# Performance work log

Measured on AMD Instinct MI355X. Metric: run time of the kernel, lower is better.

## Reference

```python
import jax, jax.numpy as jnp
import numpy as np

NUM_SEGMENTS = 8
SHIFT_DIV = 4
DEFORM_GROUPS = 2


def conv1d(x, w, b):
    # x: [N, C, T], w: [O, I, K], padding=1 (same)
    y = jax.lax.conv_general_dilated(x, w, window_strides=(1,), padding=[(1, 1)],
                                     dimension_numbers=('NCH', 'OIH', 'NCH'))
    return y + b[None, :, None]


def linear_sampler(data, offset, weight):
    # data: [N, T, C, H, W]; offset: [N, 1] or [N, T]; weight: [N, T]
    n, t = data.shape[0], data.shape[1]
    location = jnp.arange(1, t + 1, dtype=data.dtype)          # [T]
    off = offset + location                                    # [N, T]
    f = jnp.floor(off).astype(jnp.int32)
    o0 = jnp.clip(f, 0, t + 1)
    o1 = jnp.clip(f + 1, 0, t + 1)
    pad = jnp.pad(data, ((0, 0), (1, 1), (0, 0), (0, 0), (0, 0)))  # [N, T+2, C, H, W]
    d0 = jnp.take_along_axis(pad, o0[:, :, None, None, None], axis=1)
    d1 = jnp.take_along_axis(pad, o1[:, :, None, None, None], axis=1)
    w0 = (1.0 - (off - o0.astype(data.dtype)))[:, :, None, None, None]
    return (w0 * d0 + (1.0 - w0) * d1) * weight[:, :, None, None, None]


def setup_inputs() -> dict:
    key = jax.random.key(0)
    ks = jax.random.split(key, 8)
    n, c, h, w = 64, 256, 56, 56
    ns = NUM_SEGMENTS
    in_ch = c // SHIFT_DIV  # 64, channels fed to offset/weight nets
    x = jax.random.normal(ks[0], (n, c, h, w), dtype=jnp.float32)
    s = 0.05
    return {
        'x': x,
        'conv_off_w': jax.random.normal(ks[1], (1, in_ch, 3), jnp.float32) * s,
        'conv_off_b': jnp.zeros((1,), jnp.float32),
        'fc1_w': jax.random.normal(ks[2], (ns, ns), jnp.float32) * s,
        'fc1_b': jnp.zeros((ns,), jnp.float32),
        'fc2_w': jax.random.normal(ks[3], (DEFORM_GROUPS, ns), jnp.float32) * s,
        'fc2_b': jnp.full((DEFORM_GROUPS,), 0.5108, jnp.float32),
        'conv_wt_w': jax.random.normal(ks[4], (DEFORM_GROUPS, in_ch, 3), jnp.float32) * s,
        'conv_wt_b': jnp.zeros((DEFORM_GROUPS,), jnp.float32),
    }


def reference(x, conv_off_w, conv_off_b, fc1_w, fc1_b, fc2_w, fc2_b, conv_wt_w, conv_wt_b):
    n, c, h, w = x.shape
    ns = NUM_SEGMENTS
    nb = n // ns
    num_folds = c // SHIFT_DIV
    x_unchanged = x[:, num_folds:]
    xd = x[:, :num_folds].reshape(nb, ns, num_folds, h, w)
    # global spatial pool -> [nb, num_folds, ns]
    x_pooled = xd.mean(axis=(3, 4)).transpose(0, 2, 1)
    # OffsetNet: conv1d -> fc1 -> relu -> fc2 -> 4*(sigmoid-0.5)
    xo = conv1d(x_pooled, conv_off_w, conv_off_b).reshape(nb, ns)
    xo = jax.nn.relu(xo @ fc1_w.T + fc1_b)
    xo = xo @ fc2_w.T + fc2_b                       # [nb, groups]
    x_offset = (4.0 * (jax.nn.sigmoid(xo) - 0.5)).reshape(nb, 1, DEFORM_GROUPS)
    # WeightNet: conv1d -> 2*sigmoid
    xw = conv1d(x_pooled, conv_wt_w, conv_wt_b)     # [nb, groups, ns]
    x_weight = 2.0 * jax.nn.sigmoid(xw.transpose(0, 2, 1))  # [nb, ns, groups]
    x_offset = -x_offset
    fi = num_folds // DEFORM_GROUPS // 2
    parts = []
    for i in range(DEFORM_GROUPS):
        parts.append(linear_sampler(xd[:, :, i * fi:(i + 1) * fi],
                                    x_offset[:, :, i], x_weight[:, :, i]))
    for i in range(DEFORM_GROUPS):
        p = i + DEFORM_GROUPS
        parts.append(linear_sampler(xd[:, :, p * fi:(p + 1) * fi],
                                    -x_offset[:, :, i], x_weight[:, :, i]))
    x_shift = jnp.concatenate(parts, axis=2)        # [nb, ns, num_folds, h, w]
    x_shift = x_shift.reshape(n, num_folds, h, w)
    x_out = jnp.concatenate([x_shift, x_unchanged], axis=1)
    return x_out, x_offset, x_weight
```

## Files before the change

kernel.cpp:

```cpp
#include <hip/hip_runtime.h>
#include <hip/hip_bf16.h>


#define HW4      784
#define N_TOT    64
#define C_TOT    256
#define FOLDS    64
#define MAIN_OUT (64u*256u*784u)
#define OFF_OUT  51380224
#define WT_OUT   51380240

typedef float v4f __attribute__((ext_vector_type(4)));

__global__ __launch_bounds__(256) void pool_kernel(const v4f* __restrict__ x,
                                                   float* __restrict__ pool) {
    const int p = blockIdx.x;
    const int n = p >> 6, f = p & 63;
    const v4f* base = x + (size_t)(n * C_TOT + f) * HW4;
    float s = 0.f;
    for (int i = threadIdx.x; i < HW4; i += 256) {
        v4f v = base[i];
        s += (v.x + v.y) + (v.z + v.w);
    }
    for (int m = 32; m >= 1; m >>= 1) s += __shfl_xor(s, m, 64);
    __shared__ float ls[4];
    if ((threadIdx.x & 63) == 0) ls[threadIdx.x >> 6] = s;
    __syncthreads();
    if (threadIdx.x == 0)
        pool[p] = (ls[0] + ls[1] + ls[2] + ls[3]) * (1.0f / 3136.0f);
}

__global__ __launch_bounds__(256) void mid_kernel(const float* __restrict__ pool,
    const float* __restrict__ cow, const float* __restrict__ cob,
    const float* __restrict__ f1w, const float* __restrict__ f1b,
    const float* __restrict__ f2w, const float* __restrict__ f2b,
    const float* __restrict__ cww, const float* __restrict__ cwb,
    float* __restrict__ out_off, float* __restrict__ out_wt,
    v4f* __restrict__ param) {
    __shared__ float sp[4096];
    __shared__ float sxo[64];
    __shared__ float sxw[128];
    __shared__ float sy[64];
    __shared__ float soff[16];
    __shared__ float swt[128];
    const int t = threadIdx.x;
    for (int i = t; i < 4096; i += 256) sp[i] = pool[i];
    __syncthreads();
    if (t < 64) {
        const int b = t >> 3, s = t & 7;
        float acc = cob[0];
        for (int f = 0; f < 64; ++f) {
            float vm = (s >= 1) ? sp[(b*8 + s - 1)*64 + f] : 0.f;
            float v0 = sp[(b*8 + s)*64 + f];
            float vp = (s <= 6) ? sp[(b*8 + s + 1)*64 + f] : 0.f;
            acc += cow[f*3+0]*vm + cow[f*3+1]*v0 + cow[f*3+2]*vp;
        }
        sxo[t] = acc;
    } else if (t < 192) {
        const int j = t - 64;
        const int b = j >> 4, g = (j >> 3) & 1, s = j & 7;
        float acc = cwb[g];
        for (int f = 0; f < 64; ++f) {
            float vm = (s >= 1) ? sp[(b*8 + s - 1)*64 + f] : 0.f;
            float v0 = sp[(b*8 + s)*64 + f];
            float vp = (s <= 6) ? sp[(b*8 + s + 1)*64 + f] : 0.f;
            const float* w = &cww[(g*64 + f)*3];
            acc += w[0]*vm + w[1]*v0 + w[2]*vp;
        }
        sxw[j] = acc;
    }
    __syncthreads();
    if (t < 64) {
        const int b = t >> 3, j = t & 7;
        float acc = f1b[j];
        for (int s = 0; s < 8; ++s) acc += sxo[b*8+s] * f1w[j*8+s];
        sy[t] = fmaxf(acc, 0.f);
    } else if (t < 192) {
        const int q = t - 64;
        const int b = q >> 4, s = (q >> 1) & 7, g = q & 1;
        float wv = 2.f / (1.f + expf(-sxw[b*16 + g*8 + s]));
        swt[b*16 + s*2 + g] = wv;
        out_wt[b*16 + s*2 + g] = wv;
    }
    __syncthreads();
    if (t < 16) {
        const int b = t >> 1, g = t & 1;
        float acc = f2b[g];
        for (int j = 0; j < 8; ++j) acc += sy[b*8+j] * f2w[g*8+j];
        float off = -(4.f * (1.f / (1.f + expf(-acc)) - 0.5f));
        soff[b*2+g] = off;
        out_off[b*2+g] = off;
    }
    __syncthreads();
    {
        const int i = t & 3, s = (t >> 2) & 7, b = t >> 5;
        const int g = i & 1;
        float d = soff[b*2+g];
        if (i >= 2) d = -d;
        float off = d + (float)(s + 1);
        int fi = (int)floorf(off);
        int o0 = min(max(fi, 0), 9);
        int o1 = min(max(fi + 1, 0), 9);
        float w0 = 1.f - (off - (float)o0);
        int n0 = (o0 >= 1 && o0 <= 8) ? (b*8 + o0 - 1) : -1;
        int n1 = (o1 >= 1 && o1 <= 8) ? (b*8 + o1 - 1) : -1;
        float wt = swt[b*16 + s*2 + g];
        v4f pv;
        pv.x = __int_as_float(n0);
        pv.y = __int_as_float(n1);
        pv.z = w0;
        pv.w = wt;
        param[(b*8 + s)*4 + i] = pv;
    }
}

__global__ __launch_bounds__(256) void out_kernel(const v4f* __restrict__ x,
                                                  const v4f* __restrict__ param,
                                                  v4f* __restrict__ out) {
    const unsigned stride = gridDim.x * blockDim.x;
    for (unsigned idx = blockIdx.x * blockDim.x + threadIdx.x; idx < MAIN_OUT;
         idx += stride) {
        const unsigned plane = idx / 784u;
        const unsigned r     = idx - plane * 784u;
        const unsigned c     = plane & 255u;
        v4f v;
        if (c >= 64u) {
            v = __builtin_nontemporal_load(&x[idx]);
        } else {
            const unsigned n = plane >> 8;
            const v4f p = param[n*4u + (c >> 4)];
            const int n0 = __float_as_int(p.x);
            const int n1 = __float_as_int(p.y);
            const float w0 = p.z, wt = p.w, w1 = 1.f - w0;
            v4f a = (v4f)(0.f);
            v4f b = (v4f)(0.f);
            if (n0 >= 0) a = x[((unsigned)n0 * 256u + c) * 784u + r];
            if (n1 >= 0) b = x[((unsigned)n1 * 256u + c) * 784u + r];
            v = (w0*a + w1*b) * wt;
        }
        __builtin_nontemporal_store(v, &out[idx]);
    }
}

extern "C" void kernel_launch(void* const* d_in, const int* in_sizes, int n_in,
                              void* d_out, int out_size, void* d_ws, size_t ws_size,
                              hipStream_t stream) {
    const float* x   = (const float*)d_in[0];
    const float* cow = (const float*)d_in[1];
    const float* cob = (const float*)d_in[2];
    const float* f1w = (const float*)d_in[3];
    const float* f1b = (const float*)d_in[4];
    const float* f2w = (const float*)d_in[5];
    const float* f2b = (const float*)d_in[6];
    const float* cww = (const float*)d_in[7];
    const float* cwb = (const float*)d_in[8];
    float* out = (float*)d_out;

    float* pool  = (float*)d_ws;
    v4f*   param = (v4f*)((char*)d_ws + 4096 * sizeof(float));

    pool_kernel<<<4096, 256, 0, stream>>>((const v4f*)x, pool);
    mid_kernel<<<1, 256, 0, stream>>>(pool, cow, cob, f1w, f1b, f2w, f2b,
                                      cww, cwb, out + OFF_OUT, out + WT_OUT, param);
    out_kernel<<<2048, 256, 0, stream>>>((const v4f*)x, param, (v4f*)out);
}
```

Measured before the change: 365.9 us.

## Fuse pool, param, and output kernels into one cooperative kernel with grid syncs

Merges the three launches (pooling, small MLP/param computation, output sampling/copy) into a single cooperative kernel of 512 blocks separated by grid-wide syncs. Pooling now uses one wavefront per channel plane instead of one block, and the output loop drops the nontemporal load/store hints. This removes launch gaps and lets the x reads in the output phase hit cache from pooling, but the tail is serialized on block 0 while all other blocks wait, and the grid is smaller than before.

```diff
diff --git a/kernel.cpp b/kernel.cpp
--- a/kernel.cpp
+++ b/kernel.cpp
@@ -1,151 +1,159 @@
 #include <hip/hip_runtime.h>
-#include <hip/hip_bf16.h>
+#include <hip/hip_cooperative_groups.h>
 
 
+typedef float v4f __attribute__((ext_vector_type(4)));
+
 #define HW4      784
-#define N_TOT    64
-#define C_TOT    256
-#define FOLDS    64
 #define MAIN_OUT (64u*256u*784u)
 #define OFF_OUT  51380224
 #define WT_OUT   51380240
 
-typedef float v4f __attribute__((ext_vector_type(4)));
+namespace cg = cooperative_groups;
 
-__global__ __launch_bounds__(256) void pool_kernel(const v4f* __restrict__ x,
-                                                   float* __restrict__ pool) {
-    const int p = blockIdx.x;
-    const int n = p >> 6, f = p & 63;
-    const v4f* base = x + (size_t)(n * C_TOT + f) * HW4;
-    float s = 0.f;
-    for (int i = threadIdx.x; i < HW4; i += 256) {
-        v4f v = base[i];
-        s += (v.x + v.y) + (v.z + v.w);
-    }
-    for (int m = 32; m >= 1; m >>= 1) s += __shfl_xor(s, m, 64);
-    __shared__ float ls[4];
-    if ((threadIdx.x & 63) == 0) ls[threadIdx.x >> 6] = s;
-    __syncthreads();
-    if (threadIdx.x == 0)
-        pool[p] = (ls[0] + ls[1] + ls[2] + ls[3]) * (1.0f / 3136.0f);
-}
-
-__global__ __launch_bounds__(256) void mid_kernel(const float* __restrict__ pool,
+__global__ __launch_bounds__(256, 2) void fused_kernel(
+    const v4f* __restrict__ x,
     const float* __restrict__ cow, const float* __restrict__ cob,
     const float* __restrict__ f1w, const float* __restrict__ f1b,
     const float* __restrict__ f2w, const float* __restrict__ f2b,
     const float* __restrict__ cww, const float* __restrict__ cwb,
-    float* __restrict__ out_off, float* __restrict__ out_wt,
-    v4f* __restrict__ param) {
+    float* __restrict__ out,
+    float* __restrict__ pool,
+    v4f* __restrict__ param)
+{
+    cg::grid_group grid = cg::this_grid();
+    const int t    = threadIdx.x;
+    const int lane = t & 63;
+
+    {
+        const int wv = (blockIdx.x << 2) | (t >> 6);
+        #pragma unroll
+        for (int k = 0; k < 2; ++k) {
+            const int p = wv + k * 2048;
+            const int n = p >> 6, f = p & 63;
+            const v4f* base = x + (size_t)(n * 256 + f) * HW4;
+            float s = 0.f;
+            for (int i = lane; i < HW4; i += 64) {
+                v4f v = base[i];
+                s += (v.x + v.y) + (v.z + v.w);
+            }
+            #pragma unroll
+            for (int m = 32; m >= 1; m >>= 1) s += __shfl_xor(s, m, 64);
+            if (lane == 0) pool[p] = s * (1.0f / 3136.0f);
+        }
+    }
+    grid.sync();
+
     __shared__ float sp[4096];
     __shared__ float sxo[64];
     __shared__ float sxw[128];
     __shared__ float sy[64];
     __shared__ float soff[16];
     __shared__ float swt[128];
-    const int t = threadIdx.x;
-    for (int i = t; i < 4096; i += 256) sp[i] = pool[i];
-    __syncthreads();
-    if (t < 64) {
-        const int b = t >> 3, s = t & 7;
-        float acc = cob[0];
-        for (int f = 0; f < 64; ++f) {
-            float vm = (s >= 1) ? sp[(b*8 + s - 1)*64 + f] : 0.f;
-            float v0 = sp[(b*8 + s)*64 + f];
-            float vp = (s <= 6) ? sp[(b*8 + s + 1)*64 + f] : 0.f;
-            acc += cow[f*3+0]*vm + cow[f*3+1]*v0 + cow[f*3+2]*vp;
+    if (blockIdx.x == 0) {
+        for (int i = t; i < 4096; i += 256) sp[i] = pool[i];
+        __syncthreads();
+        if (t < 64) {
+            const int b = t >> 3, s = t & 7;
+            float acc = cob[0];
+            for (int f = 0; f < 64; ++f) {
+                float vm = (s >= 1) ? sp[(b*8 + s - 1)*64 + f] : 0.f;
+                float v0 = sp[(b*8 + s)*64 + f];
+                float vp = (s <= 6) ? sp[(b*8 + s + 1)*64 + f] : 0.f;
+                acc += cow[f*3+0]*vm + cow[f*3+1]*v0 + cow[f*3+2]*vp;
+            }
+            sxo[t] = acc;
+        } else if (t < 192) {
+            const int j = t - 64;
+            const int b = j >> 4, g = (j >> 3) & 1, s = j & 7;
+            float acc = cwb[g];
+            for (int f = 0; f < 64; ++f) {
+                float vm = (s >= 1) ? sp[(b*8 + s - 1)*64 + f] : 0.f;
+                float v0 = sp[(b*8 + s)*64 + f];
+                float vp = (s <= 6) ? sp[(b*8 + s + 1)*64 + f] : 0.f;
+                const float* w = &cww[(g*64 + f)*3];
+                acc += w[0]*vm + w[1]*v0 + w[2]*vp;
+            }
+            sxw[j] = acc;
         }
-        sxo[t] = acc;
-    } else if (t < 192) {
-        const int j = t - 64;
-        const int b = j >> 4, g = (j >> 3) & 1, s = j & 7;
-        float acc = cwb[g];
-        for (int f = 0; f < 64; ++f) {
-            float vm = (s >= 1) ? sp[(b*8 + s - 1)*64 + f] : 0.f;
-            float v0 = sp[(b*8 + s)*64 + f];
-            float vp = (s <= 6) ? sp[(b*8 + s + 1)*64 + f] : 0.f;
-            const float* w = &cww[(g*64 + f)*3];
-            acc += w[0]*vm + w[1]*v0 + w[2]*vp;
+        __syncthreads();
+        if (t < 64) {
+            const int b = t >> 3, j = t & 7;
+            float acc = f1b[j];
+            for (int s = 0; s < 8; ++s) acc += sxo[b*8+s] * f1w[j*8+s];
+            sy[t] = fmaxf(acc, 0.f);
+        } else if (t < 192) {
+            const int q = t - 64;
+            const int b = q >> 4, s = (q >> 1) & 7, g = q & 1;
+            float wv = 2.f / (1.f + expf(-sxw[b*16 + g*8 + s]));
+            swt[b*16 + s*2 + g] = wv;
+            out[WT_OUT + b*16 + s*2 + g] = wv;
         }
-        sxw[j] = acc;
+        __syncthreads();
+        if (t < 16) {
+            const int b = t >> 1, g = t & 1;
+            float acc = f2b[g];
+            for (int j = 0; j < 8; ++j) acc += sy[b*8+j] * f2w[g*8+j];
+            float off = -(4.f * (1.f / (1.f + expf(-acc)) - 0.5f));
+            soff[b*2+g] = off;
+            out[OFF_OUT + b*2+g] = off;
+        }
+        __syncthreads();
+        {
+            const int i = t & 3, s = (t >> 2) & 7, b = t >> 5;
+            const int g = i & 1;
+            float d = soff[b*2+g];
+            if (i >= 2) d = -d;
+            float off = d + (float)(s + 1);
+            int fi = (int)floorf(off);
+            int o0 = min(max(fi, 0), 9);
+            int o1 = min(max(fi + 1, 0), 9);
+            float w0 = 1.f - (off - (float)o0);
+            int n0 = (o0 >= 1 && o0 <= 8) ? (b*8 + o0 - 1) : -1;
+            int n1 = (o1 >= 1 && o1 <= 8) ? (b*8 + o1 - 1) : -1;
+            float wt = swt[b*16 + s*2 + g];
+            v4f pv;
+            pv.x = __int_as_float(n0);
+            pv.y = __int_as_float(n1);
+            pv.z = w0;
+            pv.w = wt;
+            param[(b*8 + s)*4 + i] = pv;
+        }
     }
-    __syncthreads();
-    if (t < 64) {
-        const int b = t >> 3, j = t & 7;
-        float acc = f1b[j];
-        for (int s = 0; s < 8; ++s) acc += sxo[b*8+s] * f1w[j*8+s];
-        sy[t] = fmaxf(acc, 0.f);
-    } else if (t < 192) {
-        const int q = t - 64;
-        const int b = q >> 4, s = (q >> 1) & 7, g = q & 1;
-        float wv = 2.f / (1.f + expf(-sxw[b*16 + g*8 + s]));
-        swt[b*16 + s*2 + g] = wv;
-        out_wt[b*16 + s*2 + g] = wv;
-    }
-    __syncthreads();
-    if (t < 16) {
-        const int b = t >> 1, g = t & 1;
-        float acc = f2b[g];
-        for (int j = 0; j < 8; ++j) acc += sy[b*8+j] * f2w[g*8+j];
-        float off = -(4.f * (1.f / (1.f + expf(-acc)) - 0.5f));
-        soff[b*2+g] = off;
-        out_off[b*2+g] = off;
-    }
-    __syncthreads();
+    grid.sync();
+
     {
-        const int i = t & 3, s = (t >> 2) & 7, b = t >> 5;
-        const int g = i & 1;
-        float d = soff[b*2+g];
-        if (i >= 2) d = -d;
-        float off = d + (float)(s + 1);
-        int fi = (int)floorf(off);
-        int o0 = min(max(fi, 0), 9);
-        int o1 = min(max(fi + 1, 0), 9);
-        float w0 = 1.f - (off - (float)o0);
-        int n0 = (o0 >= 1 && o0 <= 8) ? (b*8 + o0 - 1) : -1;
-        int n1 = (o1 >= 1 && o1 <= 8) ? (b*8 + o1 - 1) : -1;
-        float wt = swt[b*16 + s*2 + g];
-        v4f pv;
-        pv.x = __int_as_float(n0);
-        pv.y = __int_as_float(n1);
-        pv.z = w0;
-        pv.w = wt;
-        param[(b*8 + s)*4 + i] = pv;
-    }
-}
-
-__global__ __launch_bounds__(256) void out_kernel(const v4f* __restrict__ x,
-                                                  const v4f* __restrict__ param,
-                                                  v4f* __restrict__ out) {
-    const unsigned stride = gridDim.x * blockDim.x;
-    for (unsigned idx = blockIdx.x * blockDim.x + threadIdx.x; idx < MAIN_OUT;
-         idx += stride) {
-        const unsigned plane = idx / 784u;
-        const unsigned r     = idx - plane * 784u;
-        const unsigned c     = plane & 255u;
-        v4f v;
-        if (c >= 64u) {
-            v = __builtin_nontemporal_load(&x[idx]);
-        } else {
-            const unsigned n = plane >> 8;
-            const v4f p = param[n*4u + (c >> 4)];
-            const int n0 = __float_as_int(p.x);
-            const int n1 = __float_as_int(p.y);
-            const float w0 = p.z, wt = p.w, w1 = 1.f - w0;
-            v4f a = (v4f)(0.f);
-            v4f b = (v4f)(0.f);
-            if (n0 >= 0) a = x[((unsigned)n0 * 256u + c) * 784u + r];
-            if (n1 >= 0) b = x[((unsigned)n1 * 256u + c) * 784u + r];
-            v = (w0*a + w1*b) * wt;
+        const unsigned stride = gridDim.x * blockDim.x;
+        v4f* outv = (v4f*)out;
+        for (unsigned idx = blockIdx.x * blockDim.x + t; idx < MAIN_OUT;
+             idx += stride) {
+            const unsigned plane = idx / 784u;
+            const unsigned r     = idx - plane * 784u;
+            const unsigned c     = plane & 255u;
+            v4f v;
+            if (c >= 64u) {
+                v = x[idx];
+            } else {
+                const unsigned n = plane >> 8;
+                const v4f p = param[n*4u + (c >> 4)];
+                const int n0 = __float_as_int(p.x);
+                const int n1 = __float_as_int(p.y);
+                const float w0 = p.z, wt = p.w, w1 = 1.f - w0;
+                v4f a = (v4f)(0.f);
+                v4f b = (v4f)(0.f);
+                if (n0 >= 0) a = x[((unsigned)n0 * 256u + c) * 784u + r];
+                if (n1 >= 0) b = x[((unsigned)n1 * 256u + c) * 784u + r];
+                v = (w0*a + w1*b) * wt;
+            }
+            outv[idx] = v;
         }
-        __builtin_nontemporal_store(v, &out[idx]);
     }
 }
 
 extern "C" void kernel_launch(void* const* d_in, const int* in_sizes, int n_in,
                               void* d_out, int out_size, void* d_ws, size_t ws_size,
                               hipStream_t stream) {
-    const float* x   = (const float*)d_in[0];
+    const v4f*   x   = (const v4f*)d_in[0];
     const float* cow = (const float*)d_in[1];
     const float* cob = (const float*)d_in[2];
     const float* f1w = (const float*)d_in[3];
@@ -159,8 +167,11 @@
     float* pool  = (float*)d_ws;
     v4f*   param = (v4f*)((char*)d_ws + 4096 * sizeof(float));
 
-    pool_kernel<<<4096, 256, 0, stream>>>((const v4f*)x, pool);
-    mid_kernel<<<1, 256, 0, stream>>>(pool, cow, cob, f1w, f1b, f2w, f2b,
-                                      cww, cwb, out + OFF_OUT, out + WT_OUT, param);
-    out_kernel<<<2048, 256, 0, stream>>>((const v4f*)x, param, (v4f*)out);
+    void* args[12] = {
+        (void*)&x,   (void*)&cow, (void*)&cob, (void*)&f1w, (void*)&f1b,
+        (void*)&f2w, (void*)&f2b, (void*)&cww, (void*)&cwb,
+        (void*)&out, (void*)&pool, (void*)&param
+    };
+    hipLaunchCooperativeKernel((void*)fused_kernel, dim3(512), dim3(256),
+                               args, 0, stream);
 }
```

Result: slower. 494.9 us (+35.3%).
